# Performance work log

Hardware: AMD Instinct MI355X
Metric: run time of the kernel (lower is better)

The kernel has to match this reference:

```python
import jax, jax.numpy as jnp
import numpy as np

EPS = 1e-5
MIN_NORM = 1e-10

def _norm(x):
    return jnp.sqrt(jnp.clip(jnp.sum(x * x, axis=-1, keepdims=True), MIN_NORM, None))

def _proj(x):
    # clip points to the open unit Poincare ball
    n = _norm(x)
    max_n = 1.0 - EPS
    return jnp.where(n > max_n, x * (max_n / n), x)

def _artanh(x):
    return jnp.arctanh(jnp.clip(x, -1.0 + EPS, 1.0 - EPS))

def mob_add(u, v):
    uv = jnp.sum(u * v, axis=-1, keepdims=True)
    u2 = jnp.sum(u * u, axis=-1, keepdims=True)
    v2 = jnp.sum(v * v, axis=-1, keepdims=True)
    num = (1.0 + 2.0 * uv + v2) * u + (1.0 - u2) * v
    den = 1.0 + 2.0 * uv + u2 * v2
    return _proj(num / jnp.maximum(den, MIN_NORM))

def mob_mat_mul(M, x):
    # M: [Din, Dout], x: [B, Din] on the ball. Ganea Mobius matvec.
    x = _proj(x)
    Mx = x @ M
    x_n = _norm(x)
    Mx_n = _norm(Mx)
    return _proj(jnp.tanh(Mx_n / x_n * _artanh(x_n)) * (Mx / Mx_n))

def log_map_zero(y):
    n = _norm(y)
    return _artanh(n) * y / n

def exp_map_zero(v):
    n = _norm(v)
    return _proj(jnp.tanh(n) * v / n)

def mob_pointwise_prod(x, u):
    # coordinate-wise scale of hyperbolic x by gate u, in the tangent space at 0
    return exp_map_zero(log_map_zero(x) * u)

def _transition(W, h, U, x, b):
    Wh = mob_mat_mul(W, h)
    Ux = mob_mat_mul(U, x)
    return mob_add(mob_add(Wh, Ux), b)

def setup_inputs() -> dict:
    B, I, H = 2048, 1024, 1024
    Din, Dh = 2 * I, 2 * H
    k = (1.0 / H) ** 0.5
    key = jax.random.key(0)
    ks = jax.random.split(key, 8)
    return {
        "hyp_x": jax.random.normal(ks[0], (B, Din), jnp.float32) * 0.01,
        "hidden": jax.random.normal(ks[1], (B, Dh), jnp.float32) * 0.01,
        "w_z": jax.random.uniform(ks[2], (Dh, Dh), jnp.float32, -k, k),
        "w_r": jax.random.uniform(ks[3], (Dh, Dh), jnp.float32, -k, k),
        "w_h": jax.random.uniform(ks[4], (Dh, Dh), jnp.float32, -k, k),
        "u_z": jax.random.uniform(ks[5], (Din, Dh), jnp.float32, -k, k),
        "u_r": jax.random.uniform(ks[6], (Din, Dh), jnp.float32, -k, k),
        "b_z": jnp.zeros((Dh,), jnp.float32),
        "b_r": jnp.zeros((Dh,), jnp.float32),
        "b_h": jnp.zeros((Dh,), jnp.float32),
    }

def reference(hyp_x, hidden, w_z, w_r, w_h, u_z, u_r, b_z, b_r, b_h):
    hyp_x = _proj(hyp_x)
    hidden = _proj(hidden)
    z = jax.nn.sigmoid(log_map_zero(_transition(w_z, hidden, u_z, hyp_x, b_z)))
    r = jax.nn.sigmoid(log_map_zero(_transition(w_r, hidden, u_r, hyp_x, b_r)))
    r_point_h = mob_pointwise_prod(hidden, r)
    # NOTE: original source uses u_r (not u_h) here; replicated faithfully.
    h_tilde = _transition(w_h, r_point_h, u_r, hyp_x, b_h)
    minus_h_oplus_htilde = mob_add(-hidden, h_tilde)
    new_h = mob_add(hidden, mob_pointwise_prod(minus_h_oplus_htilde, z))
    return new_h
```

## Files before the change

kernel.cpp:

```cpp
#include <hip/hip_runtime.h>
#include <hip/hip_bf16.h>
#include <math.h>

#define EPS 1e-5f
#define MAXN (1.0f - EPS)
#define MINN 1e-10f

constexpr int D = 2048;
constexpr int LPT = 8;

typedef unsigned short u16;
typedef __bf16 bf16x8 __attribute__((ext_vector_type(8)));
typedef float floatx4 __attribute__((ext_vector_type(4)));


__device__ __forceinline__ u16 f2bf(float f) {
    union { float f; unsigned u; } v; v.f = f;
    unsigned r = v.u + 0x7FFFu + ((v.u >> 16) & 1u);
    return (u16)(r >> 16);
}

__device__ __forceinline__ float artanh_(float x) {
    x = fminf(fmaxf(x, -1.0f + EPS), 1.0f - EPS);
    return 0.5f * logf((1.0f + x) / (1.0f - x));
}

__device__ __forceinline__ float sigmoid_(float x) {
    return 1.0f / (1.0f + expf(-x));
}

__device__ __forceinline__ void gl_lds16(const u16* g, u16* l) {
    __builtin_amdgcn_global_load_lds(
        (const __attribute__((address_space(1))) unsigned int*)g,
        (__attribute__((address_space(3))) unsigned int*)l, 16, 0, 0);
}

__device__ __forceinline__ float block_sum(float v, float* sbuf) {
    #pragma unroll
    for (int off = 32; off >= 1; off >>= 1) v += __shfl_xor(v, off, 64);
    int w = threadIdx.x >> 6;
    __syncthreads();
    if ((threadIdx.x & 63) == 0) sbuf[w] = v;
    __syncthreads();
    return sbuf[0] + sbuf[1] + sbuf[2] + sbuf[3];
}

__device__ __forceinline__ void mmm_finish(float sum2, float g, float* coef, float* onorm) {
    float mxn = sqrtf(fmaxf(sum2, MINN));
    float tt  = tanhf(mxn * g);
    float on  = fminf(tt, MAXN);
    *coef = on / mxn;
    *onorm = on;
}

__device__ __forceinline__ float mob_add_frag(float* u, const float* v,
                                              float u2, float v2, float* sbuf) {
    float duv = 0.f;
    #pragma unroll
    for (int i = 0; i < LPT; ++i) duv += u[i] * v[i];
    duv = block_sum(duv, sbuf);
    float cu  = 1.f + 2.f * duv + v2;
    float cv  = 1.f - u2;
    float den = fmaxf(1.f + 2.f * duv + u2 * v2, MINN);
    float s2 = 0.f;
    #pragma unroll
    for (int i = 0; i < LPT; ++i) {
        float nm = cu * u[i] + cv * v[i];
        u[i] = nm;
        s2 += nm * nm;
    }
    s2 = block_sum(s2, sbuf);
    float n  = sqrtf(fmaxf(s2 / (den * den), MINN));
    float sc = ((n > MAXN) ? MAXN / n : 1.f) / den;
    #pragma unroll
    for (int i = 0; i < LPT; ++i) u[i] *= sc;
    return fminf(n, MAXN);
}


struct TransBatch { const float* W[5]; u16* Wt[5]; };

__global__ __launch_bounds__(256) void wtrans(TransBatch tb) {
    const float* W = tb.W[blockIdx.z];
    u16* Wt = tb.Wt[blockIdx.z];
    __shared__ float tile[64 * 65];
    int n0 = blockIdx.x * 64, k0 = blockIdx.y * 64;
    int t = threadIdx.x;

    int lr = t >> 4, lc = (t & 15) * 4;
    #pragma unroll
    for (int p = 0; p < 4; ++p) {
        int r = lr + p * 16;
        float4 v = *(const float4*)(W + (size_t)(k0 + r) * D + n0 + lc);
        tile[r * 65 + lc + 0] = v.x;
        tile[r * 65 + lc + 1] = v.y;
        tile[r * 65 + lc + 2] = v.z;
        tile[r * 65 + lc + 3] = v.w;
    }
    __syncthreads();

    int wn = t >> 3, ws = (t & 7) * 8;
    #pragma unroll
    for (int p = 0; p < 2; ++p) {
        int n = wn + p * 32;
        u16 pk[8];
        #pragma unroll
        for (int j = 0; j < 8; ++j) pk[j] = f2bf(tile[(ws + j) * 65 + n]);
        *(uint4*)(Wt + (size_t)(n0 + n) * D + k0 + ws) = *(uint4*)pk;
    }
}


__global__ __launch_bounds__(256) void prep(
    const float* __restrict__ hx, const float* __restrict__ h,
    u16* __restrict__ hx_bf, u16* __restrict__ h_bf,
    float* __restrict__ h_proj, float* __restrict__ g_x, float* __restrict__ g_h) {
    __shared__ float sbuf[4];
    int b = blockIdx.x, t = threadIdx.x;
    size_t off = (size_t)b * D;

    {
        float xv[LPT]; float s = 0.f;
        #pragma unroll
        for (int i = 0; i < LPT; ++i) { xv[i] = hx[off + t + 256 * i]; s += xv[i] * xv[i]; }
        float n = sqrtf(fmaxf(block_sum(s, sbuf), MINN));
        float scale = (n > MAXN) ? MAXN / n : 1.0f;
        float xn = fminf(n, MAXN);
        #pragma unroll
        for (int i = 0; i < LPT; ++i) hx_bf[off + t + 256 * i] = f2bf(xv[i] * scale);
        if (t == 0) g_x[b] = artanh_(xn) / xn;
    }
    {
        float xv[LPT]; float s = 0.f;
        #pragma unroll
        for (int i = 0; i < LPT; ++i) { xv[i] = h[off + t + 256 * i]; s += xv[i] * xv[i]; }
        float n = sqrtf(fmaxf(block_sum(s, sbuf), MINN));
        float scale = (n > MAXN) ? MAXN / n : 1.0f;
        float xn = fminf(n, MAXN);
        #pragma unroll
        for (int i = 0; i < LPT; ++i) {
            float pv = xv[i] * scale;
            h_bf[off + t + 256 * i] = f2bf(pv);
            h_proj[off + t + 256 * i] = pv;
        }
        if (t == 0) g_h[b] = artanh_(xn) / xn;
    }
}


struct GemmBatch { const u16* A[4]; const u16* W[4]; float* C[4]; int koff[4]; };

template<int KLEN>
__global__ __launch_bounds__(256) void gemm_bt(GemmBatch gb) {
    int z = blockIdx.z;
    const u16* __restrict__ A = gb.A[z];
    const u16* __restrict__ W = gb.W[z];
    float* __restrict__ C = gb.C[z];
    int koff = gb.koff[z];

    __shared__ u16 As[128 * 64];
    __shared__ u16 Ws[128 * 64];

    int t = threadIdx.x;
    int wave = t >> 6, lane = t & 63;
    int wr = wave >> 1, wc = wave & 1;
    int quad = lane >> 4, l16 = lane & 15;
    int brow = blockIdx.y * 128, bcol = blockIdx.x * 128;

    int srow = 32 * wave + (lane >> 3);
    int sseg = (lane & 7) ^ ((lane >> 3) & 7);
    const u16* pa = A + (size_t)(brow + srow) * D + koff + sseg * 8;
    const u16* pw = W + (size_t)(bcol + srow) * D + koff + sseg * 8;
    u16* lbA = &As[wave * 2048];
    u16* lbW = &Ws[wave * 2048];

    floatx4 acc[4][4];
    #pragma unroll
    for (int i = 0; i < 4; ++i)
        #pragma unroll
        for (int j = 0; j < 4; ++j)
            #pragma unroll
            for (int e = 0; e < 4; ++e) acc[i][j][e] = 0.f;

    int xsw = l16 & 7;

    for (int k0 = 0; k0 < KLEN; k0 += 64) {
        __syncthreads();
        #pragma unroll
        for (int i = 0; i < 4; ++i) {
            gl_lds16(pa + (size_t)(8 * i) * D + k0, lbA + i * 512);
            gl_lds16(pw + (size_t)(8 * i) * D + k0, lbW + i * 512);
        }
        __syncthreads();

        #pragma unroll
        for (int kk = 0; kk < 2; ++kk) {
            bf16x8 af[4], bfv[4];
            int ps = ((kk * 4 + quad) ^ xsw) * 8;
            #pragma unroll
            for (int i = 0; i < 4; ++i)
                af[i] = *(const bf16x8*)(&As[(wr * 64 + i * 16 + l16) * 64 + ps]);
            #pragma unroll
            for (int j = 0; j < 4; ++j)
                bfv[j] = *(const bf16x8*)(&Ws[(wc * 64 + j * 16 + l16) * 64 + ps]);
            #pragma unroll
            for (int i = 0; i < 4; ++i)
                #pragma unroll
                for (int j = 0; j < 4; ++j)
                    acc[i][j] = __builtin_amdgcn_mfma_f32_16x16x32_bf16(af[i], bfv[j], acc[i][j], 0, 0, 0);
        }
    }

    #pragma unroll
    for (int i = 0; i < 4; ++i) {
        #pragma unroll
        for (int j = 0; j < 4; ++j) {
            int row = brow + wr * 64 + i * 16 + quad * 4;
            int col = bcol + wc * 64 + j * 16 + l16;
            #pragma unroll
            for (int r = 0; r < 4; ++r)
                C[(size_t)(row + r) * D + col] = acc[i][j][r];
        }
    }
}


__global__ __launch_bounds__(256) void mid_kernel(
    const float* __restrict__ c_wz, const float* __restrict__ c_uz,
    const float* __restrict__ c_wr, const float* __restrict__ c_ur,
    const float* __restrict__ h_proj,
    const float* __restrict__ g_x, const float* __restrict__ g_h,
    const float* __restrict__ b_z, const float* __restrict__ b_r,
    float* __restrict__ z_out, float* __restrict__ uxr_out,
    u16* __restrict__ rph_bf, float* __restrict__ g_rph) {
    __shared__ float sbuf[4];
    int b = blockIdx.x, t = threadIdx.x;
    size_t off = (size_t)b * D;

    float wz[LPT], uz[LPT], wr2[LPT], ur2[LPT], hp[LPT], bz[LPT], br[LPT], zz[LPT];
    float swz = 0, suz = 0, swr = 0, sur = 0;
    #pragma unroll
    for (int i = 0; i < LPT; ++i) {
        int c = t + 256 * i;
        wz[i]  = c_wz[off + c];  swz += wz[i] * wz[i];
        uz[i]  = c_uz[off + c];  suz += uz[i] * uz[i];
        wr2[i] = c_wr[off + c];  swr += wr2[i] * wr2[i];
        ur2[i] = c_ur[off + c];  sur += ur2[i] * ur2[i];
        hp[i]  = h_proj[off + c];
        bz[i]  = b_z[c];
        br[i]  = b_r[c];
    }
    float gh = g_h[b], gx = g_x[b];
    swz = block_sum(swz, sbuf);
    suz = block_sum(suz, sbuf);
    swr = block_sum(swr, sbuf);
    sur = block_sum(sur, sbuf);

    float cwz, nwz, cuz, nuz, cwr, nwr, cur, nur;
    mmm_finish(swz, gh, &cwz, &nwz);
    mmm_finish(suz, gx, &cuz, &nuz);
    mmm_finish(swr, gh, &cwr, &nwr);
    mmm_finish(sur, gx, &cur, &nur);
    #pragma unroll
    for (int i = 0; i < LPT; ++i) {
        wz[i] *= cwz; uz[i] *= cuz; wr2[i] *= cwr; ur2[i] *= cur;
    }

    float sbz = 0, sbr2 = 0;
    #pragma unroll
    for (int i = 0; i < LPT; ++i) { sbz += bz[i] * bz[i]; sbr2 += br[i] * br[i]; }
    sbz  = block_sum(sbz, sbuf);
    sbr2 = block_sum(sbr2, sbuf);

    float n1 = mob_add_frag(wz, uz, nwz * nwz, nuz * nuz, sbuf);
    float n2 = mob_add_frag(wz, bz, n1 * n1, sbz, sbuf);
    float gz = artanh_(n2) / n2;
    #pragma unroll
    for (int i = 0; i < LPT; ++i) {
        zz[i] = sigmoid_(gz * wz[i]);
        z_out[off + t + 256 * i] = zz[i];
    }

    float n1r = mob_add_frag(wr2, ur2, nwr * nwr, nur * nur, sbuf);
    float n2r = mob_add_frag(wr2, br, n1r * n1r, sbr2, sbuf);
    float gr = artanh_(n2r) / n2r;
    #pragma unroll
    for (int i = 0; i < LPT; ++i) br[i] = sigmoid_(gr * wr2[i]);

    float sv = 0.f;
    #pragma unroll
    for (int i = 0; i < LPT; ++i) {
        float v = gh * hp[i] * br[i];
        wz[i] = v;
        sv += v * v;
    }
    sv = block_sum(sv, sbuf);
    float nv = sqrtf(fmaxf(sv, MINN));
    float th = fminf(tanhf(nv), MAXN);
    float cr = th / nv;
    #pragma unroll
    for (int i = 0; i < LPT; ++i) {
        rph_bf[off + t + 256 * i] = f2bf(wz[i] * cr);
        uxr_out[off + t + 256 * i] = ur2[i];
    }
    if (t == 0) g_rph[b] = artanh_(th) / th;
}


__global__ __launch_bounds__(256) void fin_kernel(
    const float* __restrict__ p0, const float* __restrict__ p1,
    const float* __restrict__ p2, const float* __restrict__ p3,
    const float* __restrict__ uxr,
    const float* __restrict__ z_in, const float* __restrict__ h_proj,
    const float* __restrict__ g_rph, const float* __restrict__ b_h,
    float* __restrict__ out) {
    __shared__ float sbuf[4];
    int b = blockIdx.x, t = threadIdx.x;
    size_t off = (size_t)b * D;

    float wh[LPT], ux[LPT], zz[LPT], hp[LPT], bh[LPT];
    float swh = 0, sux = 0, shp = 0, sbh = 0;
    #pragma unroll
    for (int i = 0; i < LPT; ++i) {
        int c = t + 256 * i;
        wh[i] = p0[off + c] + p1[off + c] + p2[off + c] + p3[off + c];
        swh += wh[i] * wh[i];
        ux[i] = uxr[off + c];   sux += ux[i] * ux[i];
        zz[i] = z_in[off + c];
        hp[i] = h_proj[off + c]; shp += hp[i] * hp[i];
        bh[i] = b_h[c];         sbh += bh[i] * bh[i];
    }
    swh = block_sum(swh, sbuf);
    sux = block_sum(sux, sbuf);
    shp = block_sum(shp, sbuf);
    sbh = block_sum(sbh, sbuf);

    float cwh, nwh;
    mmm_finish(swh, g_rph[b], &cwh, &nwh);
    #pragma unroll
    for (int i = 0; i < LPT; ++i) wh[i] *= cwh;

    float n1  = mob_add_frag(wh, ux, nwh * nwh, sux, sbuf);
    float nht = mob_add_frag(wh, bh, n1 * n1, sbh, sbuf);

    #pragma unroll
    for (int i = 0; i < LPT; ++i) ux[i] = -hp[i];
    float nm = mob_add_frag(ux, wh, shp, nht * nht, sbuf);

    float lm = artanh_(nm) / nm;
    float sv = 0.f;
    #pragma unroll
    for (int i = 0; i < LPT; ++i) {
        float v = lm * ux[i] * zz[i];
        ux[i] = v;
        sv += v * v;
    }
    sv = block_sum(sv, sbuf);
    float nv = sqrtf(fmaxf(sv, MINN));
    float th = fminf(tanhf(nv), MAXN);
    float ce = th / nv;
    #pragma unroll
    for (int i = 0; i < LPT; ++i) ux[i] *= ce;

    mob_add_frag(hp, ux, shp, th * th, sbuf);
    #pragma unroll
    for (int i = 0; i < LPT; ++i) out[off + t + 256 * i] = hp[i];
}


extern "C" void kernel_launch(void* const* d_in, const int* in_sizes, int n_in,
                              void* d_out, int out_size, void* d_ws, size_t ws_size,
                              hipStream_t stream) {
    const float* hyp_x  = (const float*)d_in[0];
    const float* hidden = (const float*)d_in[1];
    const float* w_z = (const float*)d_in[2];
    const float* w_r = (const float*)d_in[3];
    const float* w_h = (const float*)d_in[4];
    const float* u_z = (const float*)d_in[5];
    const float* u_r = (const float*)d_in[6];
    const float* b_z = (const float*)d_in[7];
    const float* b_r = (const float*)d_in[8];
    const float* b_h = (const float*)d_in[9];
    float* out = (float*)d_out;

    int B = in_sizes[1] / D;

    char* ws = (char*)d_ws;
    size_t o = 0;
    auto alloc = [&](size_t bytes) -> void* {
        void* p = ws + o;
        o += (bytes + 255) & ~(size_t)255;
        return p;
    };
    u16* wt[5];
    for (int i = 0; i < 5; ++i) wt[i] = (u16*)alloc((size_t)D * D * 2);
    u16* hx_bf   = (u16*)alloc((size_t)B * D * 2);
    u16* h_bf    = (u16*)alloc((size_t)B * D * 2);
    float* h_proj = (float*)alloc((size_t)B * D * 4);
    float* g_x   = (float*)alloc((size_t)B * 4);
    float* g_h   = (float*)alloc((size_t)B * 4);
    float* g_rph = (float*)alloc((size_t)B * 4);
    float* c0 = (float*)alloc((size_t)B * D * 4);
    float* c1 = (float*)alloc((size_t)B * D * 4);
    float* c2 = (float*)alloc((size_t)B * D * 4);
    float* c3 = (float*)alloc((size_t)B * D * 4);
    float* z_buf = (float*)alloc((size_t)B * D * 4);
    float* uxr   = (float*)alloc((size_t)B * D * 4);
    u16* rph     = (u16*)alloc((size_t)B * D * 2);

    TransBatch tb;
    tb.W[0] = w_z; tb.W[1] = w_r; tb.W[2] = w_h; tb.W[3] = u_z; tb.W[4] = u_r;
    for (int i = 0; i < 5; ++i) tb.Wt[i] = wt[i];
    wtrans<<<dim3(D / 64, D / 64, 5), 256, 0, stream>>>(tb);

    prep<<<dim3(B), 256, 0, stream>>>(hyp_x, hidden, hx_bf, h_bf, h_proj, g_x, g_h);

    GemmBatch g1;
    g1.A[0] = h_bf;  g1.W[0] = wt[0]; g1.C[0] = c0;
    g1.A[1] = hx_bf; g1.W[1] = wt[3]; g1.C[1] = c1;
    g1.A[2] = h_bf;  g1.W[2] = wt[1]; g1.C[2] = c2;
    g1.A[3] = hx_bf; g1.W[3] = wt[4]; g1.C[3] = c3;
    for (int i = 0; i < 4; ++i) g1.koff[i] = 0;
    gemm_bt<2048><<<dim3(D / 128, B / 128, 4), 256, 0, stream>>>(g1);

    mid_kernel<<<dim3(B), 256, 0, stream>>>(c0, c1, c2, c3, h_proj, g_x, g_h,
                                            b_z, b_r, z_buf, uxr, rph, g_rph);

    GemmBatch g2;
    float* cb[4] = {c0, c1, c2, c3};
    for (int s = 0; s < 4; ++s) {
        g2.A[s] = rph; g2.W[s] = wt[2]; g2.C[s] = cb[s]; g2.koff[s] = s * 512;
    }
    gemm_bt<512><<<dim3(D / 128, B / 128, 4), 256, 0, stream>>>(g2);

    fin_kernel<<<dim3(B), 256, 0, stream>>>(c0, c1, c2, c3, uxr, z_buf, h_proj,
                                            g_rph, b_h, out);
}
```

Baseline: 338.0 us.

## Store intermediates in bf16, vectorize row kernels, batch block reductions

```diff
diff --git a/kernel.cpp b/kernel.cpp
--- a/kernel.cpp
+++ b/kernel.cpp
@@ -7,7 +7,6 @@
 #define MINN 1e-10f
 
 constexpr int D = 2048;
-constexpr int LPT = 8;
 
 typedef unsigned short u16;
 typedef __bf16 bf16x8 __attribute__((ext_vector_type(8)));
@@ -20,6 +19,37 @@
     return (u16)(r >> 16);
 }
 
+__device__ __forceinline__ float bf2f(u16 b) {
+    union { unsigned u; float f; } v; v.u = ((unsigned)b) << 16; return v.f;
+}
+
+__device__ __forceinline__ void load_bf8(const u16* p, float* d) {
+    uint4 r = *(const uint4*)p;
+    unsigned w[4] = {r.x, r.y, r.z, r.w};
+    #pragma unroll
+    for (int i = 0; i < 4; ++i) {
+        d[2 * i]     = bf2f((u16)(w[i] & 0xFFFFu));
+        d[2 * i + 1] = bf2f((u16)(w[i] >> 16));
+    }
+}
+
+__device__ __forceinline__ void store_bf8(u16* p, const float* s) {
+    u16 pk[8];
+    #pragma unroll
+    for (int i = 0; i < 8; ++i) pk[i] = f2bf(s[i]);
+    *(uint4*)p = *(const uint4*)pk;
+}
+
+__device__ __forceinline__ void load_f8(const float* p, float* d) {
+    *(float4*)(d)     = *(const float4*)(p);
+    *(float4*)(d + 4) = *(const float4*)(p + 4);
+}
+
+__device__ __forceinline__ void store_f8(float* p, const float* s) {
+    *(float4*)(p)     = *(const float4*)(s);
+    *(float4*)(p + 4) = *(const float4*)(s + 4);
+}
+
 __device__ __forceinline__ float artanh_(float x) {
     x = fminf(fmaxf(x, -1.0f + EPS), 1.0f - EPS);
     return 0.5f * logf((1.0f + x) / (1.0f - x));
@@ -35,14 +65,22 @@
         (__attribute__((address_space(3))) unsigned int*)l, 16, 0, 0);
 }
 
-__device__ __forceinline__ float block_sum(float v, float* sbuf) {
-    #pragma unroll
-    for (int off = 32; off >= 1; off >>= 1) v += __shfl_xor(v, off, 64);
+template<int N>
+__device__ __forceinline__ void block_sums(float* v, float* sbuf) {
+    #pragma unroll
+    for (int n = 0; n < N; ++n)
+        #pragma unroll
+        for (int off = 32; off >= 1; off >>= 1) v[n] += __shfl_xor(v[n], off, 64);
     int w = threadIdx.x >> 6;
     __syncthreads();
-    if ((threadIdx.x & 63) == 0) sbuf[w] = v;
+    if ((threadIdx.x & 63) == 0) {
+        #pragma unroll
+        for (int n = 0; n < N; ++n) sbuf[w * N + n] = v[n];
+    }
     __syncthreads();
-    return sbuf[0] + sbuf[1] + sbuf[2] + sbuf[3];
+    #pragma unroll
+    for (int n = 0; n < N; ++n)
+        v[n] = sbuf[n] + sbuf[N + n] + sbuf[2 * N + n] + sbuf[3 * N + n];
 }
 
 __device__ __forceinline__ void mmm_finish(float sum2, float g, float* coef, float* onorm) {
@@ -53,27 +91,16 @@
     *onorm = on;
 }
 
-__device__ __forceinline__ float mob_add_frag(float* u, const float* v,
-                                              float u2, float v2, float* sbuf) {
-    float duv = 0.f;
-    #pragma unroll
-    for (int i = 0; i < LPT; ++i) duv += u[i] * v[i];
-    duv = block_sum(duv, sbuf);
+__device__ __forceinline__ float mob_apply(float* u, const float* v,
+                                           float u2, float v2, float duv) {
     float cu  = 1.f + 2.f * duv + v2;
     float cv  = 1.f - u2;
     float den = fmaxf(1.f + 2.f * duv + u2 * v2, MINN);
-    float s2 = 0.f;
-    #pragma unroll
-    for (int i = 0; i < LPT; ++i) {
-        float nm = cu * u[i] + cv * v[i];
-        u[i] = nm;
-        s2 += nm * nm;
-    }
-    s2 = block_sum(s2, sbuf);
-    float n  = sqrtf(fmaxf(s2 / (den * den), MINN));
-    float sc = ((n > MAXN) ? MAXN / n : 1.f) / den;
-    #pragma unroll
-    for (int i = 0; i < LPT; ++i) u[i] *= sc;
+    float s2  = cu * cu * u2 + 2.f * cu * cv * duv + cv * cv * v2;
+    float n   = sqrtf(fmaxf(s2 / (den * den), MINN));
+    float sc  = ((n > MAXN) ? MAXN / n : 1.f) / den;
+    #pragma unroll
+    for (int i = 0; i < 8; ++i) u[i] = sc * (cu * u[i] + cv * v[i]);
     return fminf(n, MAXN);
 }
 
@@ -114,48 +141,43 @@
 __global__ __launch_bounds__(256) void prep(
     const float* __restrict__ hx, const float* __restrict__ h,
     u16* __restrict__ hx_bf, u16* __restrict__ h_bf,
-    float* __restrict__ h_proj, float* __restrict__ g_x, float* __restrict__ g_h) {
-    __shared__ float sbuf[4];
+    float* __restrict__ g_x, float* __restrict__ g_h) {
+    __shared__ float sbuf[8];
     int b = blockIdx.x, t = threadIdx.x;
-    size_t off = (size_t)b * D;
-
-    {
-        float xv[LPT]; float s = 0.f;
-        #pragma unroll
-        for (int i = 0; i < LPT; ++i) { xv[i] = hx[off + t + 256 * i]; s += xv[i] * xv[i]; }
-        float n = sqrtf(fmaxf(block_sum(s, sbuf), MINN));
-        float scale = (n > MAXN) ? MAXN / n : 1.0f;
-        float xn = fminf(n, MAXN);
-        #pragma unroll
-        for (int i = 0; i < LPT; ++i) hx_bf[off + t + 256 * i] = f2bf(xv[i] * scale);
-        if (t == 0) g_x[b] = artanh_(xn) / xn;
-    }
-    {
-        float xv[LPT]; float s = 0.f;
-        #pragma unroll
-        for (int i = 0; i < LPT; ++i) { xv[i] = h[off + t + 256 * i]; s += xv[i] * xv[i]; }
-        float n = sqrtf(fmaxf(block_sum(s, sbuf), MINN));
-        float scale = (n > MAXN) ? MAXN / n : 1.0f;
-        float xn = fminf(n, MAXN);
-        #pragma unroll
-        for (int i = 0; i < LPT; ++i) {
-            float pv = xv[i] * scale;
-            h_bf[off + t + 256 * i] = f2bf(pv);
-            h_proj[off + t + 256 * i] = pv;
-        }
-        if (t == 0) g_h[b] = artanh_(xn) / xn;
-    }
-}
-
-
-struct GemmBatch { const u16* A[4]; const u16* W[4]; float* C[4]; int koff[4]; };
-
-template<int KLEN>
+    size_t off = (size_t)b * D + t * 8;
+
+    float xv[8], hv[8];
+    load_f8(hx + off, xv);
+    load_f8(h + off, hv);
+    float s[2] = {0.f, 0.f};
+    #pragma unroll
+    for (int i = 0; i < 8; ++i) { s[0] += xv[i] * xv[i]; s[1] += hv[i] * hv[i]; }
+    block_sums<2>(s, sbuf);
+
+    float nx = sqrtf(fmaxf(s[0], MINN));
+    float scx = (nx > MAXN) ? MAXN / nx : 1.0f;
+    float nh = sqrtf(fmaxf(s[1], MINN));
+    float sch = (nh > MAXN) ? MAXN / nh : 1.0f;
+    #pragma unroll
+    for (int i = 0; i < 8; ++i) { xv[i] *= scx; hv[i] *= sch; }
+    store_bf8(hx_bf + off, xv);
+    store_bf8(h_bf + off, hv);
+    if (t == 0) {
+        float xn = fminf(nx, MAXN), hn = fminf(nh, MAXN);
+        g_x[b] = artanh_(xn) / xn;
+        g_h[b] = artanh_(hn) / hn;
+    }
+}
+
+
+struct GemmBatch { const u16* A[4]; const u16* W[4]; void* C[4]; int koff[4]; };
+
+template<int KLEN, typename CT>
 __global__ __launch_bounds__(256) void gemm_bt(GemmBatch gb) {
     int z = blockIdx.z;
     const u16* __restrict__ A = gb.A[z];
     const u16* __restrict__ W = gb.W[z];
-    float* __restrict__ C = gb.C[z];
+    CT* __restrict__ C = (CT*)gb.C[z];
     int koff = gb.koff[z];
 
     __shared__ u16 As[128 * 64];
@@ -218,91 +240,95 @@
             int row = brow + wr * 64 + i * 16 + quad * 4;
             int col = bcol + wc * 64 + j * 16 + l16;
             #pragma unroll
-            for (int r = 0; r < 4; ++r)
-                C[(size_t)(row + r) * D + col] = acc[i][j][r];
+            for (int r = 0; r < 4; ++r) {
+                float val = acc[i][j][r];
+                if constexpr (sizeof(CT) == 2)
+                    C[(size_t)(row + r) * D + col] = (CT)f2bf(val);
+                else
+                    C[(size_t)(row + r) * D + col] = (CT)val;
+            }
         }
     }
 }
 
 
 __global__ __launch_bounds__(256) void mid_kernel(
-    const float* __restrict__ c_wz, const float* __restrict__ c_uz,
-    const float* __restrict__ c_wr, const float* __restrict__ c_ur,
-    const float* __restrict__ h_proj,
+    const u16* __restrict__ c_wz, const u16* __restrict__ c_uz,
+    const u16* __restrict__ c_wr, const u16* __restrict__ c_ur,
+    const u16* __restrict__ h_bf,
     const float* __restrict__ g_x, const float* __restrict__ g_h,
     const float* __restrict__ b_z, const float* __restrict__ b_r,
-    float* __restrict__ z_out, float* __restrict__ uxr_out,
+    float* __restrict__ z_out, u16* __restrict__ uxr_out,
     u16* __restrict__ rph_bf, float* __restrict__ g_rph) {
-    __shared__ float sbuf[4];
+    __shared__ float sbuf[24];
     int b = blockIdx.x, t = threadIdx.x;
-    size_t off = (size_t)b * D;
-
-    float wz[LPT], uz[LPT], wr2[LPT], ur2[LPT], hp[LPT], bz[LPT], br[LPT], zz[LPT];
-    float swz = 0, suz = 0, swr = 0, sur = 0;
-    #pragma unroll
-    for (int i = 0; i < LPT; ++i) {
-        int c = t + 256 * i;
-        wz[i]  = c_wz[off + c];  swz += wz[i] * wz[i];
-        uz[i]  = c_uz[off + c];  suz += uz[i] * uz[i];
-        wr2[i] = c_wr[off + c];  swr += wr2[i] * wr2[i];
-        ur2[i] = c_ur[off + c];  sur += ur2[i] * ur2[i];
-        hp[i]  = h_proj[off + c];
-        bz[i]  = b_z[c];
-        br[i]  = b_r[c];
-    }
+    size_t off = (size_t)b * D + t * 8;
+    int cbase = t * 8;
+
+    float wz[8], uz[8], wr2[8], ur2[8], hp[8], bz[8], br[8];
+    load_bf8(c_wz + off, wz);
+    load_bf8(c_uz + off, uz);
+    load_bf8(c_wr + off, wr2);
+    load_bf8(c_ur + off, ur2);
+    load_bf8(h_bf + off, hp);
+    load_f8(b_z + cbase, bz);
+    load_f8(b_r + cbase, br);
+
+    float s[6] = {0, 0, 0, 0, 0, 0};
+    #pragma unroll
+    for (int i = 0; i < 8; ++i) {
+        s[0] += wz[i] * wz[i];  s[1] += uz[i] * uz[i];
+        s[2] += wr2[i] * wr2[i]; s[3] += ur2[i] * ur2[i];
+        s[4] += bz[i] * bz[i];  s[5] += br[i] * br[i];
+    }
+    block_sums<6>(s, sbuf);
     float gh = g_h[b], gx = g_x[b];
-    swz = block_sum(swz, sbuf);
-    suz = block_sum(suz, sbuf);
-    swr = block_sum(swr, sbuf);
-    sur = block_sum(sur, sbuf);
 
     float cwz, nwz, cuz, nuz, cwr, nwr, cur, nur;
-    mmm_finish(swz, gh, &cwz, &nwz);
-    mmm_finish(suz, gx, &cuz, &nuz);
-    mmm_finish(swr, gh, &cwr, &nwr);
-    mmm_finish(sur, gx, &cur, &nur);
-    #pragma unroll
-    for (int i = 0; i < LPT; ++i) {
+    mmm_finish(s[0], gh, &cwz, &nwz);
+    mmm_finish(s[1], gx, &cuz, &nuz);
+    mmm_finish(s[2], gh, &cwr, &nwr);
+    mmm_finish(s[3], gx, &cur, &nur);
+    #pragma unroll
+    for (int i = 0; i < 8; ++i) {
         wz[i] *= cwz; uz[i] *= cuz; wr2[i] *= cwr; ur2[i] *= cur;
     }
-
-    float sbz = 0, sbr2 = 0;
-    #pragma unroll
-    for (int i = 0; i < LPT; ++i) { sbz += bz[i] * bz[i]; sbr2 += br[i] * br[i]; }
-    sbz  = block_sum(sbz, sbuf);
-    sbr2 = block_sum(sbr2, sbuf);
-
-    float n1 = mob_add_frag(wz, uz, nwz * nwz, nuz * nuz, sbuf);
-    float n2 = mob_add_frag(wz, bz, n1 * n1, sbz, sbuf);
-    float gz = artanh_(n2) / n2;
-    #pragma unroll
-    for (int i = 0; i < LPT; ++i) {
+    float sbz = s[4], sbr2 = s[5];
+
+    float d[2] = {0.f, 0.f};
+    #pragma unroll
+    for (int i = 0; i < 8; ++i) { d[0] += wz[i] * uz[i]; d[1] += wr2[i] * ur2[i]; }
+    block_sums<2>(d, sbuf);
+    float n1z = mob_apply(wz, uz, nwz * nwz, nuz * nuz, d[0]);
+    float n1r = mob_apply(wr2, ur2, nwr * nwr, nur * nur, d[1]);
+
+    d[0] = 0.f; d[1] = 0.f;
+    #pragma unroll
+    for (int i = 0; i < 8; ++i) { d[0] += wz[i] * bz[i]; d[1] += wr2[i] * br[i]; }
+    block_sums<2>(d, sbuf);
+    float n2z = mob_apply(wz, bz, n1z * n1z, sbz, d[0]);
+    float n2r = mob_apply(wr2, br, n1r * n1r, sbr2, d[1]);
+
+    float gz = artanh_(n2z) / n2z;
+    float gr = artanh_(n2r) / n2r;
+    float zz[8], v[8];
+    float sv = 0.f;
+    #pragma unroll
+    for (int i = 0; i < 8; ++i) {
         zz[i] = sigmoid_(gz * wz[i]);
-        z_out[off + t + 256 * i] = zz[i];
-    }
-
-    float n1r = mob_add_frag(wr2, ur2, nwr * nwr, nur * nur, sbuf);
-    float n2r = mob_add_frag(wr2, br, n1r * n1r, sbr2, sbuf);
-    float gr = artanh_(n2r) / n2r;
-    #pragma unroll
-    for (int i = 0; i < LPT; ++i) br[i] = sigmoid_(gr * wr2[i]);
-
-    float sv = 0.f;
-    #pragma unroll
-    for (int i = 0; i < LPT; ++i) {
-        float v = gh * hp[i] * br[i];
-        wz[i] = v;
-        sv += v * v;
-    }
-    sv = block_sum(sv, sbuf);
+        float r = sigmoid_(gr * wr2[i]);
+        v[i] = gh * hp[i] * r;
+        sv += v[i] * v[i];
+    }
+    store_f8(z_out + off, zz);
+    block_sums<1>(&sv, sbuf);
     float nv = sqrtf(fmaxf(sv, MINN));
     float th = fminf(tanhf(nv), MAXN);
     float cr = th / nv;
     #pragma unroll
-    for (int i = 0; i < LPT; ++i) {
-        rph_bf[off + t + 256 * i] = f2bf(wz[i] * cr);
-        uxr_out[off + t + 256 * i] = ur2[i];
-    }
+    for (int i = 0; i < 8; ++i) v[i] *= cr;
+    store_bf8(rph_bf + off, v);
+    store_bf8(uxr_out + off, ur2);
     if (t == 0) g_rph[b] = artanh_(th) / th;
 }
 
@@ -310,61 +336,84 @@
 __global__ __launch_bounds__(256) void fin_kernel(
     const float* __restrict__ p0, const float* __restrict__ p1,
     const float* __restrict__ p2, const float* __restrict__ p3,
-    const float* __restrict__ uxr,
-    const float* __restrict__ z_in, const float* __restrict__ h_proj,
+    const u16* __restrict__ uxr, const float* __restrict__ z_in,
+    const u16* __restrict__ h_bf,
     const float* __restrict__ g_rph, const float* __restrict__ b_h,
     float* __restrict__ out) {
-    __shared__ float sbuf[4];
+    __shared__ float sbuf[16];
     int b = blockIdx.x, t = threadIdx.x;
-    size_t off = (size_t)b * D;
-
-    float wh[LPT], ux[LPT], zz[LPT], hp[LPT], bh[LPT];
-    float swh = 0, sux = 0, shp = 0, sbh = 0;
-    #pragma unroll
-    for (int i = 0; i < LPT; ++i) {
-        int c = t + 256 * i;
-        wh[i] = p0[off + c] + p1[off + c] + p2[off + c] + p3[off + c];
-        swh += wh[i] * wh[i];
-        ux[i] = uxr[off + c];   sux += ux[i] * ux[i];
-        zz[i] = z_in[off + c];
-        hp[i] = h_proj[off + c]; shp += hp[i] * hp[i];
-        bh[i] = b_h[c];         sbh += bh[i] * bh[i];
-    }
-    swh = block_sum(swh, sbuf);
-    sux = block_sum(sux, sbuf);
-    shp = block_sum(shp, sbuf);
-    sbh = block_sum(sbh, sbuf);
+    size_t off = (size_t)b * D + t * 8;
+    int cbase = t * 8;
+
+    float wh[8], ux[8], zz[8], hp[8], bh[8], t0[8], t1[8];
+    load_f8(p0 + off, wh);
+    load_f8(p1 + off, t0);
+    load_f8(p2 + off, t1);
+    #pragma unroll
+    for (int i = 0; i < 8; ++i) wh[i] += t0[i] + t1[i];
+    load_f8(p3 + off, t0);
+    #pragma unroll
+    for (int i = 0; i < 8; ++i) wh[i] += t0[i];
+    load_bf8(uxr + off, ux);
+    load_f8(z_in + off, zz);
+    load_bf8(h_bf + off, hp);
+    load_f8(b_h + cbase, bh);
+
+    float s[4] = {0, 0, 0, 0};
+    #pragma unroll
+    for (int i = 0; i < 8; ++i) {
+        s[0] += wh[i] * wh[i]; s[1] += ux[i] * ux[i];
+        s[2] += hp[i] * hp[i]; s[3] += bh[i] * bh[i];
+    }
+    block_sums<4>(s, sbuf);
+    float swh = s[0], sux = s[1], shp = s[2], sbh = s[3];
 
     float cwh, nwh;
     mmm_finish(swh, g_rph[b], &cwh, &nwh);
     #pragma unroll
-    for (int i = 0; i < LPT; ++i) wh[i] *= cwh;
-
-    float n1  = mob_add_frag(wh, ux, nwh * nwh, sux, sbuf);
-    float nht = mob_add_frag(wh, bh, n1 * n1, sbh, sbuf);
-
-    #pragma unroll
-    for (int i = 0; i < LPT; ++i) ux[i] = -hp[i];
-    float nm = mob_add_frag(ux, wh, shp, nht * nht, sbuf);
+    for (int i = 0; i < 8; ++i) wh[i] *= cwh;
+
+    float d = 0.f;
+    #pragma unroll
+    for (int i = 0; i < 8; ++i) d += wh[i] * ux[i];
+    block_sums<1>(&d, sbuf);
+    float n1 = mob_apply(wh, ux, nwh * nwh, sux, d);
+
+    d = 0.f;
+    #pragma unroll
+    for (int i = 0; i < 8; ++i) d += wh[i] * bh[i];
+    block_sums<1>(&d, sbuf);
+    float nht = mob_apply(wh, bh, n1 * n1, sbh, d);
+
+    #pragma unroll
+    for (int i = 0; i < 8; ++i) ux[i] = -hp[i];
+    d = 0.f;
+    #pragma unroll
+    for (int i = 0; i < 8; ++i) d += ux[i] * wh[i];
+    block_sums<1>(&d, sbuf);
+    float nm = mob_apply(ux, wh, shp, nht * nht, d);
 
     float lm = artanh_(nm) / nm;
     float sv = 0.f;
     #pragma unroll
-    for (int i = 0; i < LPT; ++i) {
+    for (int i = 0; i < 8; ++i) {
         float v = lm * ux[i] * zz[i];
         ux[i] = v;
         sv += v * v;
     }
-    sv = block_sum(sv, sbuf);
+    block_sums<1>(&sv, sbuf);
     float nv = sqrtf(fmaxf(sv, MINN));
     float th = fminf(tanhf(nv), MAXN);
     float ce = th / nv;
     #pragma unroll
-    for (int i = 0; i < LPT; ++i) ux[i] *= ce;
-
-    mob_add_frag(hp, ux, shp, th * th, sbuf);
-    #pragma unroll
-    for (int i = 0; i < LPT; ++i) out[off + t + 256 * i] = hp[i];
+    for (int i = 0; i < 8; ++i) ux[i] *= ce;
+
+    d = 0.f;
+    #pragma unroll
+    for (int i = 0; i < 8; ++i) d += hp[i] * ux[i];
+    block_sums<1>(&d, sbuf);
+    mob_apply(hp, ux, shp, th * th, d);
+    store_f8(out + off, hp);
 }
 
 
@@ -394,45 +443,48 @@
     };
     u16* wt[5];
     for (int i = 0; i < 5; ++i) wt[i] = (u16*)alloc((size_t)D * D * 2);
-    u16* hx_bf   = (u16*)alloc((size_t)B * D * 2);
-    u16* h_bf    = (u16*)alloc((size_t)B * D * 2);
-    float* h_proj = (float*)alloc((size_t)B * D * 4);
+    u16* hx_bf = (u16*)alloc((size_t)B * D * 2);
+    u16* h_bf  = (u16*)alloc((size_t)B * D * 2);
     float* g_x   = (float*)alloc((size_t)B * 4);
     float* g_h   = (float*)alloc((size_t)B * 4);
     float* g_rph = (float*)alloc((size_t)B * 4);
-    float* c0 = (float*)alloc((size_t)B * D * 4);
-    float* c1 = (float*)alloc((size_t)B * D * 4);
-    float* c2 = (float*)alloc((size_t)B * D * 4);
-    float* c3 = (float*)alloc((size_t)B * D * 4);
+    u16* cz0 = (u16*)alloc((size_t)B * D * 2);
+    u16* cz1 = (u16*)alloc((size_t)B * D * 2);
+    u16* cz2 = (u16*)alloc((size_t)B * D * 2);
+    u16* cz3 = (u16*)alloc((size_t)B * D * 2);
+    float* p0 = (float*)alloc((size_t)B * D * 4);
+    float* p1 = (float*)alloc((size_t)B * D * 4);
+    float* p2 = (float*)alloc((size_t)B * D * 4);
+    float* p3 = (float*)alloc((size_t)B * D * 4);
     float* z_buf = (float*)alloc((size_t)B * D * 4);
-    float* uxr   = (float*)alloc((size_t)B * D * 4);
-    u16* rph     = (u16*)alloc((size_t)B * D * 2);
+    u16* uxr = (u16*)alloc((size_t)B * D * 2);
+    u16* rph = (u16*)alloc((size_t)B * D * 2);
 
     TransBatch tb;
     tb.W[0] = w_z; tb.W[1] = w_r; tb.W[2] = w_h; tb.W[3] = u_z; tb.W[4] = u_r;
     for (int i = 0; i < 5; ++i) tb.Wt[i] = wt[i];
     wtrans<<<dim3(D / 64, D / 64, 5), 256, 0, stream>>>(tb);
 
-    prep<<<dim3(B), 256, 0, stream>>>(hyp_x, hidden, hx_bf, h_bf, h_proj, g_x, g_h);
+    prep<<<dim3(B), 256, 0, stream>>>(hyp_x, hidden, hx_bf, h_bf, g_x, g_h);
 
     GemmBatch g1;
-    g1.A[0] = h_bf;  g1.W[0] = wt[0]; g1.C[0] = c0;
-    g1.A[1] = hx_bf; g1.W[1] = wt[3]; g1.C[1] = c1;
-    g1.A[2] = h_bf;  g1.W[2] = wt[1]; g1.C[2] = c2;
-    g1.A[3] = hx_bf; g1.W[3] = wt[4]; g1.C[3] = c3;
+    g1.A[0] = h_bf;  g1.W[0] = wt[0]; g1.C[0] = cz0;
+    g1.A[1] = hx_bf; g1.W[1] = wt[3]; g1.C[1] = cz1;
+    g1.A[2] = h_bf;  g1.W[2] = wt[1]; g1.C[2] = cz2;
+    g1.A[3] = hx_bf; g1.W[3] = wt[4]; g1.C[3] = cz3;
     for (int i = 0; i < 4; ++i) g1.koff[i] = 0;
-    gemm_bt<2048><<<dim3(D / 128, B / 128, 4), 256, 0, stream>>>(g1);
-
-    mid_kernel<<<dim3(B), 256, 0, stream>>>(c0, c1, c2, c3, h_proj, g_x, g_h,
+    gemm_bt<2048, u16><<<dim3(D / 128, B / 128, 4), 256, 0, stream>>>(g1);
+
+    mid_kernel<<<dim3(B), 256, 0, stream>>>(cz0, cz1, cz2, cz3, h_bf, g_x, g_h,
                                             b_z, b_r, z_buf, uxr, rph, g_rph);
 
     GemmBatch g2;
-    float* cb[4] = {c0, c1, c2, c3};
+    float* pb[4] = {p0, p1, p2, p3};
     for (int s = 0; s < 4; ++s) {
-        g2.A[s] = rph; g2.W[s] = wt[2]; g2.C[s] = cb[s]; g2.koff[s] = s * 512;
-    }
-    gemm_bt<512><<<dim3(D / 128, B / 128, 4), 256, 0, stream>>>(g2);
-
-    fin_kernel<<<dim3(B), 256, 0, stream>>>(c0, c1, c2, c3, uxr, z_buf, h_proj,
+        g2.A[s] = rph; g2.W[s] = wt[2]; g2.C[s] = pb[s]; g2.koff[s] = s * 512;
+    }
+    gemm_bt<512, float><<<dim3(D / 128, B / 128, 4), 256, 0, stream>>>(g2);
+
+    fin_kernel<<<dim3(B), 256, 0, stream>>>(p0, p1, p2, p3, uxr, z_buf, h_bf,
                                             g_rph, b_h, out);
 }
```

Result: faster. 324.7 us (-3.9%).
